# Kernel tuning notes

Hardware: AMD Instinct MI355X
Metric: run time of the kernel (lower is better)

Reference implementation:

```python
import jax, jax.numpy as jnp
import numpy as np

PATCH = 3       # match_patch_size
WEIGHT = 100.0  # style_weight


def _patches(fm, p):
    """fm: [C, H, W] -> [H*W, C*p*p] patch matrix (zero-padded, centered),
    equivalent to extracting p x p patches from F.pad(fm, [pad]*4) at every pixel."""
    C, H, W = fm.shape
    pad = (p - 1) // 2
    fp = jnp.pad(fm, ((0, 0), (pad, pad), (pad, pad)))
    shifts = [fp[:, di:di + H, dj:dj + W] for di in range(p) for dj in range(p)]
    # [p*p, C, H, W] -> [p*p*C, H*W] -> [H*W, p*p*C]
    return jnp.stack(shifts, axis=0).reshape(p * p * C, H * W).T


def _masked_gram(fm, mask_full, mask_sum):
    """fm: [1, C, H, W]; gram of masked fm, normalized by sum of expanded mask."""
    C = fm.shape[1]
    f = (fm * mask_full)[0].reshape(C, -1)
    return (f @ f.T) / mask_sum


def setup_inputs() -> dict:
    key = jax.random.key(0)
    k1, k2, k3, k4 = jax.random.split(key, 4)
    shape = (1, 512, 64, 64)
    return {
        "input_fm": jax.random.normal(k1, shape, dtype=jnp.float32),
        "style_fm": jax.random.normal(k2, shape, dtype=jnp.float32),
        "content_fm": jax.random.normal(k3, shape, dtype=jnp.float32),
        "mask": jax.random.uniform(k4, (1, 1, 64, 64), dtype=jnp.float32),
    }


def reference(input_fm, style_fm, content_fm, mask):
    """StyleLossPass2 pipeline: capture_content -> capture_style_ref -> loss.
    Cross-correlation patch match (stride=1, same padding), argmax NN, gather
    matched style pixels, masked gram, MSE loss vs image gram."""
    p = PATCH
    s = style_fm[0]   # [C, H, W]
    c = content_fm[0]
    C, H, W = s.shape

    # All-pairs patch cross-correlation: score[i, j] = <content patch i, style patch j>
    Pc = _patches(c, p)          # [HW, C*p*p]
    Ps = _patches(s, p)          # [HW, C*p*p]
    score = Pc @ Ps.T            # [HW, HW]
    corr = jnp.argmax(score, axis=1)  # [HW] flat NN index per content position

    # Gather matched style pixels -> matched style feature map
    matched = s.reshape(C, -1)[:, corr].reshape(1, C, H, W)

    # mask expanded over C (torch: mask.expand_as(content_fm); sum over expanded mask)
    mask_full = jnp.broadcast_to(mask, input_fm.shape)
    mask_sum = jnp.sum(mask) * C

    style_matched_gram = _masked_gram(matched, mask_full, mask_sum)
    img_gram = _masked_gram(input_fm, mask_full, mask_sum)

    loss = jnp.mean((img_gram - style_matched_gram) ** 2) * WEIGHT
    return loss
```

## Files before the change

kernel.cpp:

```cpp
#include <hip/hip_runtime.h>

#define HW 4096
#define NC 512

using f32x4  = __attribute__((ext_vector_type(4))) float;
using bf16x8 = __attribute__((ext_vector_type(8))) short;
using u32x4  = __attribute__((ext_vector_type(4))) unsigned;

__device__ __forceinline__ unsigned short f2bf(float x) {
    unsigned u = __float_as_uint(x);
    unsigned r = (u + 0x7FFF + ((u >> 16) & 1)) >> 16;
    return (unsigned short)r;
}
__device__ __forceinline__ float bf2f(unsigned short v) {
    return __uint_as_float(((unsigned)v) << 16);
}

#define GLDS16(g, l) __builtin_amdgcn_global_load_lds( \
    (const __attribute__((address_space(1))) void*)(g), \
    (__attribute__((address_space(3))) void*)(l), 16, 0, 0)

__global__ __launch_bounds__(256) void transconv_kernel(const float* __restrict__ content,
                                                        const float* __restrict__ style,
                                                        unsigned short* __restrict__ cT,
                                                        unsigned short* __restrict__ sT) {
    const float* src = blockIdx.z ? style : content;
    unsigned short* dst = blockIdx.z ? sT : cT;
    __shared__ float tile[32][33];
    const int i0 = blockIdx.x * 32;
    const int c0 = blockIdx.y * 32;
    const int tx = threadIdx.x & 31, ty = threadIdx.x >> 5;
#pragma unroll
    for (int r = 0; r < 32; r += 8)
        tile[ty + r][tx] = src[(size_t)(c0 + ty + r) * HW + i0 + tx];
    __syncthreads();
#pragma unroll
    for (int r = 0; r < 32; r += 8)
        dst[(size_t)(i0 + ty + r) * NC + c0 + tx] = f2bf(tile[tx][ty + r]);
}

__global__ __launch_bounds__(256) void gemmB_mfma(const unsigned short* __restrict__ cT,
                                                  const unsigned short* __restrict__ sT,
                                                  unsigned short* __restrict__ Bb) {
    __shared__ unsigned short As[128 * 32];
    __shared__ unsigned short Bs[128 * 32];
    const int tid = threadIdx.x;
    const int wid = tid >> 6, lane = tid & 63;
    const int wr = wid >> 1, wc = wid & 1;
    const int bi = blockIdx.y * 128, bj = blockIdx.x * 128;
    f32x4 acc[4][4] = {};

    const int r0 = tid >> 2,         k80 = (tid & 3) << 3;
    const int r1 = (tid + 256) >> 2, k81 = ((tid + 256) & 3) << 3;
    unsigned short* dst0 = &As[0] + (size_t)(wid * 64) * 8;
    unsigned short* dst1 = &As[0] + (size_t)(256 + wid * 64) * 8;
    unsigned short* dstB0 = &Bs[0] + (size_t)(wid * 64) * 8;
    unsigned short* dstB1 = &Bs[0] + (size_t)(256 + wid * 64) * 8;

    for (int k0 = 0; k0 < NC; k0 += 32) {
        GLDS16(&cT[(size_t)(bi + r0) * NC + k0 + k80], dst0);
        GLDS16(&cT[(size_t)(bi + r1) * NC + k0 + k81], dst1);
        GLDS16(&sT[(size_t)(bj + r0) * NC + k0 + k80], dstB0);
        GLDS16(&sT[(size_t)(bj + r1) * NC + k0 + k81], dstB1);
        __syncthreads();
        bf16x8 a_frag[4], b_frag[4];
#pragma unroll
        for (int m = 0; m < 4; ++m)
            a_frag[m] = *(const bf16x8*)&As[(wr * 64 + m * 16 + (lane & 15)) * 32 + (lane >> 4) * 8];
#pragma unroll
        for (int n = 0; n < 4; ++n)
            b_frag[n] = *(const bf16x8*)&Bs[(wc * 64 + n * 16 + (lane & 15)) * 32 + (lane >> 4) * 8];
#pragma unroll
        for (int m = 0; m < 4; ++m)
#pragma unroll
            for (int n = 0; n < 4; ++n)
                acc[m][n] = __builtin_amdgcn_mfma_f32_16x16x32_bf16(a_frag[m], b_frag[n], acc[m][n], 0, 0, 0);
        __syncthreads();
    }
#pragma unroll
    for (int m = 0; m < 4; ++m)
#pragma unroll
        for (int n = 0; n < 4; ++n)
#pragma unroll
            for (int r = 0; r < 4; ++r) {
                int row = bi + wr * 64 + m * 16 + (lane >> 4) * 4 + r;
                int col = bj + wc * 64 + n * 16 + (lane & 15);
                Bb[(size_t)row * HW + col] = f2bf(acc[m][n][r]);
            }
}

__global__ __launch_bounds__(256) void stencilx_kernel(const unsigned short* __restrict__ Bb,
                                                       unsigned short* __restrict__ Dx) {
    const int t = threadIdx.x;
    const int r = blockIdx.x * 2 + (t >> 7);
    const int base = (t & 127) * 32;
    const int xr = r & 63;
    const bool okm = xr > 0, okp = xr < 63;
    const bool typeB = (base & 63) != 0;

    const unsigned short* rowM = Bb + (size_t)r * HW + base;
    const unsigned short* rowL = rowM - HW;
    const unsigned short* rowH = rowM + HW;

    const u32x4 Z = {0, 0, 0, 0};
    u32x4 mid[4], lov[4], hiv[4];
#pragma unroll
    for (int k = 0; k < 4; ++k) {
        mid[k] = *(const u32x4*)(rowM + 8 * k);
        lov[k] = okm ? *(const u32x4*)(rowL + 8 * k) : Z;
        hiv[k] = okp ? *(const u32x4*)(rowH + 8 * k) : Z;
    }
    float eL = (typeB && okm) ? bf2f(rowL[-1]) : 0.f;
    float eR = (!typeB && okp) ? bf2f(rowH[32]) : 0.f;

    float fm_[32], fl[32], fh[32];
#pragma unroll
    for (int k = 0; k < 4; ++k)
#pragma unroll
        for (int d = 0; d < 4; ++d) {
            unsigned dm = mid[k][d], dl = lov[k][d], dh = hiv[k][d];
            int e = k * 8 + d * 2;
            fm_[e]     = __uint_as_float(dm << 16);
            fm_[e + 1] = __uint_as_float(dm & 0xFFFF0000u);
            fl[e]      = __uint_as_float(dl << 16);
            fl[e + 1]  = __uint_as_float(dl & 0xFFFF0000u);
            fh[e]      = __uint_as_float(dh << 16);
            fh[e + 1]  = __uint_as_float(dh & 0xFFFF0000u);
        }
    unsigned short outp[32];
#pragma unroll
    for (int e = 0; e < 32; ++e) {
        float lo_v = (e == 0) ? eL : fl[e - 1];
        float hi_v = (e == 31) ? eR : fh[e + 1];
        outp[e] = f2bf(fm_[e] + lo_v + hi_v);
    }
    unsigned short* o = Dx + (size_t)r * HW + base;
#pragma unroll
    for (int k = 0; k < 4; ++k)
        *(u32x4*)(o + 8 * k) = *(u32x4*)&outp[k * 8];
}

__global__ __launch_bounds__(256) void stencily_argmax_kernel(const unsigned short* __restrict__ Dx,
                                                              int* __restrict__ corr) {
    const int i = blockIdx.x;
    const int yi = i >> 6;
    const int t = threadIdx.x;
    const bool okm = yi > 0, okp = yi < 63;
    const u32x4 Z = {0, 0, 0, 0};
    float best = -1e30f;
    int bestj = 0;
#pragma unroll
    for (int cc = 0; cc < 2; ++cc) {
        const int c0 = t * 16 + cc * 8;
        const unsigned short* pm = Dx + (size_t)i * HW + c0;
        const bool my = okm && (c0 >= 64);
        const bool mp = okp && (c0 < 4032);
        u32x4 m_ = *(const u32x4*)pm;
        u32x4 l_ = my ? *(const u32x4*)(pm - (size_t)64 * HW - 64) : Z;
        u32x4 h_ = mp ? *(const u32x4*)(pm + (size_t)64 * HW + 64) : Z;
#pragma unroll
        for (int d = 0; d < 4; ++d) {
            float s0 = __uint_as_float(m_[d] << 16) + __uint_as_float(l_[d] << 16) +
                       __uint_as_float(h_[d] << 16);
            float s1 = __uint_as_float(m_[d] & 0xFFFF0000u) + __uint_as_float(l_[d] & 0xFFFF0000u) +
                       __uint_as_float(h_[d] & 0xFFFF0000u);
            int j0 = c0 + 2 * d;
            if (s0 > best) { best = s0; bestj = j0; }
            if (s1 > best) { best = s1; bestj = j0 + 1; }
        }
    }
    __shared__ float sv[256];
    __shared__ int si[256];
    sv[t] = best; si[t] = bestj;
    __syncthreads();
    for (int off = 128; off > 0; off >>= 1) {
        if (t < off) {
            float v2 = sv[t + off]; int i2 = si[t + off];
            if (v2 > sv[t] || (v2 == sv[t] && i2 < si[t])) { sv[t] = v2; si[t] = i2; }
        }
        __syncthreads();
    }
    if (t == 0) corr[i] = si[0];
}

__global__ __launch_bounds__(256) void masksum_kernel(const float* __restrict__ mask,
                                                      float* __restrict__ scalars) {
    __shared__ float s[256];
    const int tid = threadIdx.x;
    float v = 0.f;
    for (int k = tid; k < HW; k += 256) v += mask[k];
    s[tid] = v;
    __syncthreads();
    for (int off = 128; off > 0; off >>= 1) {
        if (tid < off) s[tid] += s[tid + off];
        __syncthreads();
    }
    if (tid == 0) { scalars[0] = s[0] * 512.0f; scalars[1] = 0.f; }
}

__global__ __launch_bounds__(256) void prep_kernel(const float* __restrict__ input,
                                                   const float* __restrict__ style,
                                                   const float* __restrict__ mask,
                                                   const int* __restrict__ corr,
                                                   unsigned short* __restrict__ fib,
                                                   unsigned short* __restrict__ fmb) {
    const int g4 = (blockIdx.x * 256 + threadIdx.x) * 4;
    const int hw = g4 & 4095;
    const int c = g4 >> 12;
    float4 in = *(const float4*)&input[g4];
    float4 mk = *(const float4*)&mask[hw];
    ushort4 vi, vm;
    vi.x = f2bf(in.x * mk.x); vi.y = f2bf(in.y * mk.y);
    vi.z = f2bf(in.z * mk.z); vi.w = f2bf(in.w * mk.w);
    const float* srow = &style[(size_t)c << 12];
    vm.x = f2bf(srow[corr[hw + 0]] * mk.x);
    vm.y = f2bf(srow[corr[hw + 1]] * mk.y);
    vm.z = f2bf(srow[corr[hw + 2]] * mk.z);
    vm.w = f2bf(srow[corr[hw + 3]] * mk.w);
    *(ushort4*)&fib[g4] = vi;
    *(ushort4*)&fmb[g4] = vm;
}

__global__ __launch_bounds__(256) void gram_mfma(const unsigned short* __restrict__ fib,
                                                 const unsigned short* __restrict__ fmb,
                                                 float* __restrict__ GiP,
                                                 float* __restrict__ GmP) {
    __shared__ unsigned short Ai[128 * 32], Bi[128 * 32], Am[128 * 32], Bm[128 * 32];
    const int tid = threadIdx.x;
    const int wid = tid >> 6, lane = tid & 63;
    const int wr = wid >> 1, wc = wid & 1;
    const int bi = blockIdx.y * 128, bj = blockIdx.x * 128;
    const int kz = blockIdx.z * 256;
    f32x4 acci[4][4] = {}, accm[4][4] = {};

    const int r0 = tid >> 2,         k80 = (tid & 3) << 3;
    const int r1 = (tid + 256) >> 2, k81 = ((tid + 256) & 3) << 3;
    const size_t off0 = (size_t)(wid * 64) * 8;
    const size_t off1 = (size_t)(256 + wid * 64) * 8;

    for (int k0 = 0; k0 < 256; k0 += 32) {
        const int ka = kz + k0;
        GLDS16(&fib[(size_t)(bi + r0) * HW + ka + k80], &Ai[off0]);
        GLDS16(&fib[(size_t)(bi + r1) * HW + ka + k81], &Ai[off1]);
        GLDS16(&fib[(size_t)(bj + r0) * HW + ka + k80], &Bi[off0]);
        GLDS16(&fib[(size_t)(bj + r1) * HW + ka + k81], &Bi[off1]);
        GLDS16(&fmb[(size_t)(bi + r0) * HW + ka + k80], &Am[off0]);
        GLDS16(&fmb[(size_t)(bi + r1) * HW + ka + k81], &Am[off1]);
        GLDS16(&fmb[(size_t)(bj + r0) * HW + ka + k80], &Bm[off0]);
        GLDS16(&fmb[(size_t)(bj + r1) * HW + ka + k81], &Bm[off1]);
        __syncthreads();
        bf16x8 ai[4], bi_f[4], am[4], bm[4];
#pragma unroll
        for (int m = 0; m < 4; ++m) {
            int base = (wr * 64 + m * 16 + (lane & 15)) * 32 + (lane >> 4) * 8;
            ai[m] = *(const bf16x8*)&Ai[base];
            am[m] = *(const bf16x8*)&Am[base];
        }
#pragma unroll
        for (int n = 0; n < 4; ++n) {
            int base = (wc * 64 + n * 16 + (lane & 15)) * 32 + (lane >> 4) * 8;
            bi_f[n] = *(const bf16x8*)&Bi[base];
            bm[n] = *(const bf16x8*)&Bm[base];
        }
#pragma unroll
        for (int m = 0; m < 4; ++m)
#pragma unroll
            for (int n = 0; n < 4; ++n) {
                acci[m][n] = __builtin_amdgcn_mfma_f32_16x16x32_bf16(ai[m], bi_f[n], acci[m][n], 0, 0, 0);
                accm[m][n] = __builtin_amdgcn_mfma_f32_16x16x32_bf16(am[m], bm[n], accm[m][n], 0, 0, 0);
            }
        __syncthreads();
    }
    float* gi = GiP + (size_t)blockIdx.z * 262144;
    float* gm = GmP + (size_t)blockIdx.z * 262144;
#pragma unroll
    for (int m = 0; m < 4; ++m)
#pragma unroll
        for (int n = 0; n < 4; ++n)
#pragma unroll
            for (int r = 0; r < 4; ++r) {
                int row = bi + wr * 64 + m * 16 + (lane >> 4) * 4 + r;
                int col = bj + wc * 64 + n * 16 + (lane & 15);
                gi[(size_t)row * 512 + col] = acci[m][n][r];
                gm[(size_t)row * 512 + col] = accm[m][n][r];
            }
}

__global__ __launch_bounds__(256) void loss_kernel(const float* __restrict__ GiP,
                                                   const float* __restrict__ GmP,
                                                   float* __restrict__ scalars) {
    const int tid = threadIdx.x;
    const float inv = 1.0f / scalars[0];
    float lsum = 0.f;
    const int base = blockIdx.x * 1024;
    for (int e = base + tid; e < base + 1024; e += 256) {
        float gi = 0.f, gm = 0.f;
#pragma unroll
        for (int z = 0; z < 16; ++z) {
            gi += GiP[(size_t)z * 262144 + e];
            gm += GmP[(size_t)z * 262144 + e];
        }
        float d = (gi - gm) * inv;
        lsum = fmaf(d, d, lsum);
    }
    __shared__ float red[256];
    red[tid] = lsum;
    __syncthreads();
    for (int off = 128; off > 0; off >>= 1) {
        if (tid < off) red[tid] += red[tid + off];
        __syncthreads();
    }
    if (tid == 0) atomicAdd(&scalars[1], red[0]);
}

__global__ void finalize_kernel(const float* __restrict__ scalars,
                                float* __restrict__ out) {
    out[0] = scalars[1] * (100.0f / 262144.0f);
}

extern "C" void kernel_launch(void* const* d_in, const int* in_sizes, int n_in,
                              void* d_out, int out_size, void* d_ws, size_t ws_size,
                              hipStream_t stream) {
    (void)in_sizes; (void)n_in; (void)out_size; (void)ws_size;
    const float* input   = (const float*)d_in[0];
    const float* style   = (const float*)d_in[1];
    const float* content = (const float*)d_in[2];
    const float* mask    = (const float*)d_in[3];
    float* out = (float*)d_out;

    char* base = (char*)d_ws;
    unsigned short* Bb = (unsigned short*)base;
    unsigned short* cT = (unsigned short*)(base + (((size_t)32) << 20));
    unsigned short* sT = cT + (size_t)HW * NC;
    unsigned short* Dx = (unsigned short*)(base + (((size_t)32) << 20));
    float* GiP = (float*)base;
    float* GmP = GiP + (size_t)16 * 262144;
    unsigned short* fib = (unsigned short*)(base + (((size_t)32) << 20));
    unsigned short* fmb = fib + (size_t)NC * HW;
    int* corr = (int*)(base + (((size_t)64) << 20));
    float* scalars = (float*)(corr + HW);

    transconv_kernel<<<dim3(128, 16, 2), 256, 0, stream>>>(content, style, cT, sT);
    masksum_kernel<<<1, 256, 0, stream>>>(mask, scalars);
    gemmB_mfma<<<dim3(32, 32), 256, 0, stream>>>(cT, sT, Bb);
    stencilx_kernel<<<2048, 256, 0, stream>>>(Bb, Dx);
    stencily_argmax_kernel<<<HW, 256, 0, stream>>>(Dx, corr);
    prep_kernel<<<(NC * HW / 4) / 256, 256, 0, stream>>>(input, style, mask, corr, fib, fmb);
    gram_mfma<<<dim3(4, 4, 16), 256, 0, stream>>>(fib, fmb, GiP, GmP);
    loss_kernel<<<256, 256, 0, stream>>>(GiP, GmP, scalars);
    finalize_kernel<<<1, 1, 0, stream>>>(scalars, out);
}
```

Measured before the change: 180.8 us.

## Exploit gram symmetry, store gram difference, fuse masksum and finalize kernels

The gram kernel now computes only the upper-triangular 64x64 tiles, weighting off-diagonal tiles by two. It writes the difference between the input and matched grams instead of two separate partials, and splits K into 8 slices instead of 16. The mask-sum kernel is folded into the transpose kernel as an extra z-slice, and the finalize kernel is replaced by a last-block atomic counter in the loss kernel. This cuts launches, the gram partial traffic and redundant MFMA work, at the cost of smaller tiles with less reuse and an atomic-based completion check.

After: 166.6 us. -7.9%, faster.

```diff
diff --git a/kernel.cpp b/kernel.cpp
--- a/kernel.cpp
+++ b/kernel.cpp
@@ -23,7 +23,28 @@
 __global__ __launch_bounds__(256) void transconv_kernel(const float* __restrict__ content,
                                                         const float* __restrict__ style,
                                                         unsigned short* __restrict__ cT,
-                                                        unsigned short* __restrict__ sT) {
+                                                        unsigned short* __restrict__ sT,
+                                                        const float* __restrict__ mask,
+                                                        float* __restrict__ scalars) {
+    if (blockIdx.z == 2) {
+        if (blockIdx.x || blockIdx.y) return;
+        __shared__ float s[256];
+        const int tid = threadIdx.x;
+        float v = 0.f;
+        for (int k = tid; k < HW; k += 256) v += mask[k];
+        s[tid] = v;
+        __syncthreads();
+        for (int off = 128; off > 0; off >>= 1) {
+            if (tid < off) s[tid] += s[tid + off];
+            __syncthreads();
+        }
+        if (tid == 0) {
+            scalars[0] = s[0] * 512.0f;
+            scalars[1] = 0.f;
+            ((unsigned*)scalars)[2] = 0u;
+        }
+        return;
+    }
     const float* src = blockIdx.z ? style : content;
     unsigned short* dst = blockIdx.z ? sT : cT;
     __shared__ float tile[32][33];
@@ -181,21 +202,6 @@
         __syncthreads();
     }
     if (t == 0) corr[i] = si[0];
-}
-
-__global__ __launch_bounds__(256) void masksum_kernel(const float* __restrict__ mask,
-                                                      float* __restrict__ scalars) {
-    __shared__ float s[256];
-    const int tid = threadIdx.x;
-    float v = 0.f;
-    for (int k = tid; k < HW; k += 256) v += mask[k];
-    s[tid] = v;
-    __syncthreads();
-    for (int off = 128; off > 0; off >>= 1) {
-        if (tid < off) s[tid] += s[tid + off];
-        __syncthreads();
-    }
-    if (tid == 0) { scalars[0] = s[0] * 512.0f; scalars[1] = 0.f; }
 }
 
 __global__ __launch_bounds__(256) void prep_kernel(const float* __restrict__ input,
@@ -221,87 +227,87 @@
     *(ushort4*)&fmb[g4] = vm;
 }
 
-__global__ __launch_bounds__(256) void gram_mfma(const unsigned short* __restrict__ fib,
-                                                 const unsigned short* __restrict__ fmb,
-                                                 float* __restrict__ GiP,
-                                                 float* __restrict__ GmP) {
-    __shared__ unsigned short Ai[128 * 32], Bi[128 * 32], Am[128 * 32], Bm[128 * 32];
+__global__ __launch_bounds__(256) void gram_diff_mfma(const unsigned short* __restrict__ fib,
+                                                      const unsigned short* __restrict__ fmb,
+                                                      float* __restrict__ P) {
+    __shared__ unsigned short Ai[64 * 32], Bi[64 * 32], Am[64 * 32], Bm[64 * 32];
     const int tid = threadIdx.x;
     const int wid = tid >> 6, lane = tid & 63;
     const int wr = wid >> 1, wc = wid & 1;
-    const int bi = blockIdx.y * 128, bj = blockIdx.x * 128;
-    const int kz = blockIdx.z * 256;
-    f32x4 acci[4][4] = {}, accm[4][4] = {};
-
-    const int r0 = tid >> 2,         k80 = (tid & 3) << 3;
-    const int r1 = (tid + 256) >> 2, k81 = ((tid + 256) & 3) << 3;
-    const size_t off0 = (size_t)(wid * 64) * 8;
-    const size_t off1 = (size_t)(256 + wid * 64) * 8;
-
-    for (int k0 = 0; k0 < 256; k0 += 32) {
-        const int ka = kz + k0;
-        GLDS16(&fib[(size_t)(bi + r0) * HW + ka + k80], &Ai[off0]);
-        GLDS16(&fib[(size_t)(bi + r1) * HW + ka + k81], &Ai[off1]);
-        GLDS16(&fib[(size_t)(bj + r0) * HW + ka + k80], &Bi[off0]);
-        GLDS16(&fib[(size_t)(bj + r1) * HW + ka + k81], &Bi[off1]);
-        GLDS16(&fmb[(size_t)(bi + r0) * HW + ka + k80], &Am[off0]);
-        GLDS16(&fmb[(size_t)(bi + r1) * HW + ka + k81], &Am[off1]);
-        GLDS16(&fmb[(size_t)(bj + r0) * HW + ka + k80], &Bm[off0]);
-        GLDS16(&fmb[(size_t)(bj + r1) * HW + ka + k81], &Bm[off1]);
-        __syncthreads();
-        bf16x8 ai[4], bi_f[4], am[4], bm[4];
-#pragma unroll
-        for (int m = 0; m < 4; ++m) {
-            int base = (wr * 64 + m * 16 + (lane & 15)) * 32 + (lane >> 4) * 8;
-            ai[m] = *(const bf16x8*)&Ai[base];
-            am[m] = *(const bf16x8*)&Am[base];
-        }
-#pragma unroll
-        for (int n = 0; n < 4; ++n) {
-            int base = (wc * 64 + n * 16 + (lane & 15)) * 32 + (lane >> 4) * 8;
-            bi_f[n] = *(const bf16x8*)&Bi[base];
-            bm[n] = *(const bf16x8*)&Bm[base];
-        }
-#pragma unroll
-        for (int m = 0; m < 4; ++m)
-#pragma unroll
-            for (int n = 0; n < 4; ++n) {
-                acci[m][n] = __builtin_amdgcn_mfma_f32_16x16x32_bf16(ai[m], bi_f[n], acci[m][n], 0, 0, 0);
+    int q = blockIdx.x, ti = 0;
+    while (q >= 8 - ti) { q -= 8 - ti; ++ti; }
+    const int tj = ti + q;
+    const int row0 = ti * 64, col0 = tj * 64;
+    const int kz = blockIdx.y * 512;
+    f32x4 acci[2][2] = {}, accm[2][2] = {};
+
+    const int srow = tid >> 2, skoff = (tid & 3) << 3;
+    unsigned short* bA = &Ai[wid * 512];
+    unsigned short* bB = &Bi[wid * 512];
+    unsigned short* bC = &Am[wid * 512];
+    unsigned short* bD = &Bm[wid * 512];
+
+    for (int k0 = 0; k0 < 512; k0 += 32) {
+        const int ka = kz + k0 + skoff;
+        GLDS16(&fib[(size_t)(row0 + srow) * HW + ka], bA);
+        GLDS16(&fib[(size_t)(col0 + srow) * HW + ka], bB);
+        GLDS16(&fmb[(size_t)(row0 + srow) * HW + ka], bC);
+        GLDS16(&fmb[(size_t)(col0 + srow) * HW + ka], bD);
+        __syncthreads();
+        bf16x8 ai[2], bi_[2], am[2], bm[2];
+#pragma unroll
+        for (int m = 0; m < 2; ++m) {
+            int off = (wr * 32 + m * 16 + (lane & 15)) * 32 + (lane >> 4) * 8;
+            ai[m] = *(const bf16x8*)&Ai[off];
+            am[m] = *(const bf16x8*)&Am[off];
+        }
+#pragma unroll
+        for (int n = 0; n < 2; ++n) {
+            int off = (wc * 32 + n * 16 + (lane & 15)) * 32 + (lane >> 4) * 8;
+            bi_[n] = *(const bf16x8*)&Bi[off];
+            bm[n] = *(const bf16x8*)&Bm[off];
+        }
+#pragma unroll
+        for (int m = 0; m < 2; ++m)
+#pragma unroll
+            for (int n = 0; n < 2; ++n) {
+                acci[m][n] = __builtin_amdgcn_mfma_f32_16x16x32_bf16(ai[m], bi_[n], acci[m][n], 0, 0, 0);
                 accm[m][n] = __builtin_amdgcn_mfma_f32_16x16x32_bf16(am[m], bm[n], accm[m][n], 0, 0, 0);
             }
         __syncthreads();
     }
-    float* gi = GiP + (size_t)blockIdx.z * 262144;
-    float* gm = GmP + (size_t)blockIdx.z * 262144;
-#pragma unroll
-    for (int m = 0; m < 4; ++m)
-#pragma unroll
-        for (int n = 0; n < 4; ++n)
+    float* Pz = P + ((size_t)blockIdx.y * 36 + blockIdx.x) * 4096;
+#pragma unroll
+    for (int m = 0; m < 2; ++m)
+#pragma unroll
+        for (int n = 0; n < 2; ++n)
 #pragma unroll
             for (int r = 0; r < 4; ++r) {
-                int row = bi + wr * 64 + m * 16 + (lane >> 4) * 4 + r;
-                int col = bj + wc * 64 + n * 16 + (lane & 15);
-                gi[(size_t)row * 512 + col] = acci[m][n][r];
-                gm[(size_t)row * 512 + col] = accm[m][n][r];
+                int a_ = wr * 32 + m * 16 + (lane >> 4) * 4 + r;
+                int b_ = wc * 32 + n * 16 + (lane & 15);
+                Pz[a_ * 64 + b_] = acci[m][n][r] - accm[m][n][r];
             }
 }
 
-__global__ __launch_bounds__(256) void loss_kernel(const float* __restrict__ GiP,
-                                                   const float* __restrict__ GmP,
-                                                   float* __restrict__ scalars) {
+__global__ __launch_bounds__(256) void loss_final_kernel(const float* __restrict__ P,
+                                                         float* __restrict__ scalars,
+                                                         float* __restrict__ out) {
     const int tid = threadIdx.x;
+    const int t = blockIdx.x >> 2;
+    int q = t, ti = 0;
+    while (q >= 8 - ti) { q -= 8 - ti; ++ti; }
+    const float w = (q == 0) ? 1.0f : 2.0f;
     const float inv = 1.0f / scalars[0];
     float lsum = 0.f;
-    const int base = blockIdx.x * 1024;
-    for (int e = base + tid; e < base + 1024; e += 256) {
-        float gi = 0.f, gm = 0.f;
-#pragma unroll
-        for (int z = 0; z < 16; ++z) {
-            gi += GiP[(size_t)z * 262144 + e];
-            gm += GmP[(size_t)z * 262144 + e];
-        }
-        float d = (gi - gm) * inv;
-        lsum = fmaf(d, d, lsum);
+    const int e0 = blockIdx.x * 1024;
+#pragma unroll
+    for (int k = 0; k < 4; ++k) {
+        const int e = e0 + k * 256 + tid;
+        float g = 0.f;
+#pragma unroll
+        for (int z = 0; z < 8; ++z) g += P[(size_t)z * 147456 + e];
+        float d = g * inv;
+        lsum = fmaf(w * d, d, lsum);
     }
     __shared__ float red[256];
     red[tid] = lsum;
@@ -310,12 +316,15 @@
         if (tid < off) red[tid] += red[tid + off];
         __syncthreads();
     }
-    if (tid == 0) atomicAdd(&scalars[1], red[0]);
-}
-
-__global__ void finalize_kernel(const float* __restrict__ scalars,
-                                float* __restrict__ out) {
-    out[0] = scalars[1] * (100.0f / 262144.0f);
+    if (tid == 0) {
+        atomicAdd(&scalars[1], red[0]);
+        __threadfence();
+        unsigned old = atomicAdd(&((unsigned*)scalars)[2], 1u);
+        if (old == 143u) {
+            __threadfence();
+            out[0] = *(volatile float*)&scalars[1] * (100.0f / 262144.0f);
+        }
+    }
 }
 
 extern "C" void kernel_launch(void* const* d_in, const int* in_sizes, int n_in,
@@ -333,20 +342,17 @@
     unsigned short* cT = (unsigned short*)(base + (((size_t)32) << 20));
     unsigned short* sT = cT + (size_t)HW * NC;
     unsigned short* Dx = (unsigned short*)(base + (((size_t)32) << 20));
-    float* GiP = (float*)base;
-    float* GmP = GiP + (size_t)16 * 262144;
-    unsigned short* fib = (unsigned short*)(base + (((size_t)32) << 20));
+    unsigned short* fib = (unsigned short*)base;
     unsigned short* fmb = fib + (size_t)NC * HW;
+    float* P = (float*)(base + (((size_t)8) << 20));
     int* corr = (int*)(base + (((size_t)64) << 20));
     float* scalars = (float*)(corr + HW);
 
-    transconv_kernel<<<dim3(128, 16, 2), 256, 0, stream>>>(content, style, cT, sT);
-    masksum_kernel<<<1, 256, 0, stream>>>(mask, scalars);
+    transconv_kernel<<<dim3(128, 16, 3), 256, 0, stream>>>(content, style, cT, sT, mask, scalars);
     gemmB_mfma<<<dim3(32, 32), 256, 0, stream>>>(cT, sT, Bb);
     stencilx_kernel<<<2048, 256, 0, stream>>>(Bb, Dx);
     stencily_argmax_kernel<<<HW, 256, 0, stream>>>(Dx, corr);
     prep_kernel<<<(NC * HW / 4) / 256, 256, 0, stream>>>(input, style, mask, corr, fib, fmb);
-    gram_mfma<<<dim3(4, 4, 16), 256, 0, stream>>>(fib, fmb, GiP, GmP);
-    loss_kernel<<<256, 256, 0, stream>>>(GiP, GmP, scalars);
-    finalize_kernel<<<1, 1, 0, stream>>>(scalars, out);
-}
+    gram_diff_mfma<<<dim3(36, 8), 256, 0, stream>>>(fib, fmb, P);
+    loss_final_kernel<<<144, 256, 0, stream>>>(P, scalars, out);
+}
```
